# Optimization experiments

Measured on AMD Instinct MI355X. Metric: run time of the kernel, lower is better.

Reference implementation:

```python
import jax, jax.numpy as jnp
import numpy as np

L, D, H, DR, KF = 2, 256, 8, 64, 4   # n_layer, d_model, n_head, d_rpe, k_feedforward
B, S, T = 2, 256, 256
LN_EPS = 1e-5


def _ln(x, g, b):
    m = jnp.mean(x, -1, keepdims=True)
    v = jnp.mean((x - m) ** 2, -1, keepdims=True)
    return (x - m) * jax.lax.rsqrt(v + LN_EPS) * g + b


def _attn_rpe(q_in, kv_in, rpe, tgt_mask, wq, bq, wk, bk, wv, bv, wo, bo, wr, br):
    # RPE-biased multi-head cross attention: rpe -> (rpe_k, rpe_v) added per (src,tgt) pair.
    Bq, Sq, _ = q_in.shape
    Tk = kv_in.shape[1]
    Dh = D // H
    q = (q_in @ wq + bq).reshape(Bq, Sq, H, Dh)
    k = (kv_in @ wk + bk).reshape(Bq, Tk, H, Dh)
    v = (kv_in @ wv + bv).reshape(Bq, Tk, H, Dh)
    r = rpe @ wr + br                                   # [B,S,T,2D]
    rk, rv = jnp.split(r, 2, axis=-1)
    rk = rk.reshape(Bq, Sq, Tk, H, Dh)
    rv = rv.reshape(Bq, Sq, Tk, H, Dh)
    scale = 1.0 / np.sqrt(Dh).astype(np.float32)
    scores = (jnp.einsum('bshd,bthd->bhst', q, k)
              + jnp.einsum('bshd,bsthd->bhst', q, rk)) * scale
    scores = jnp.where(tgt_mask[:, None, None, :], -jnp.inf, scores)
    w = jax.nn.softmax(scores, axis=-1)                 # [B,H,S,T]
    out = (jnp.einsum('bhst,bthd->bshd', w, v)
           + jnp.einsum('bhst,bsthd->bshd', w, rv))
    return out.reshape(Bq, Sq, D) @ wo + bo


def _forward(src, tgt, rpe, src_padding_mask, tgt_padding_mask, p):
    for i in range(L):  # loop over n_layer (structurally distinct params)
        s2 = _ln(src, p['ln1_g'][i], p['ln1_b'][i])
        tn = _ln(tgt, p['lnt_g'][i], p['lnt_b'][i])
        a = _attn_rpe(s2, tn, rpe, tgt_padding_mask,
                      p['wq'][i], p['bq'][i], p['wk'][i], p['bk'][i],
                      p['wv'][i], p['bv'][i], p['wo'][i], p['bo'][i],
                      p['wr'][i], p['br'][i])
        src = src + a
        s2 = _ln(src, p['ln2_g'][i], p['ln2_b'][i])
        s2 = jax.nn.relu(s2 @ p['w1'][i] + p['b1'][i]) @ p['w2'][i] + p['b2'][i]
        src = src + s2
        src = jnp.where(src_padding_mask[:, :, None], 0.0, src)
    return src


def setup_inputs() -> dict:
    key = jax.random.key(0)
    ks = jax.random.split(key, 16)
    f = lambda k, shp: (0.02 * jax.random.normal(k, shp)).astype(jnp.float32)
    return {
        'src': jax.random.normal(ks[0], (B, S, D), jnp.float32),
        'tgt': jax.random.normal(ks[1], (B, T, D), jnp.float32),
        'rpe': jax.random.normal(ks[2], (B, S, T, DR), jnp.float32),
        'src_padding_mask': jax.random.bernoulli(ks[3], 0.05, (B, S)),
        'tgt_padding_mask': jax.random.bernoulli(ks[4], 0.1, (B, T)),
        'ln1_g': jnp.ones((L, D), jnp.float32), 'ln1_b': jnp.zeros((L, D), jnp.float32),
        'lnt_g': jnp.ones((L, D), jnp.float32), 'lnt_b': jnp.zeros((L, D), jnp.float32),
        'ln2_g': jnp.ones((L, D), jnp.float32), 'ln2_b': jnp.zeros((L, D), jnp.float32),
        'wq': f(ks[5], (L, D, D)), 'bq': jnp.zeros((L, D), jnp.float32),
        'wk': f(ks[6], (L, D, D)), 'bk': jnp.zeros((L, D), jnp.float32),
        'wv': f(ks[7], (L, D, D)), 'bv': jnp.zeros((L, D), jnp.float32),
        'wo': f(ks[8], (L, D, D)), 'bo': jnp.zeros((L, D), jnp.float32),
        'wr': f(ks[9], (L, DR, 2 * D)), 'br': jnp.zeros((L, 2 * D), jnp.float32),
        'w1': f(ks[10], (L, D, KF * D)), 'b1': jnp.zeros((L, KF * D), jnp.float32),
        'w2': f(ks[11], (L, KF * D, D)), 'b2': jnp.zeros((L, D), jnp.float32),
    }


def reference(src, tgt, rpe, src_padding_mask, tgt_padding_mask,
              ln1_g, ln1_b, lnt_g, lnt_b, ln2_g, ln2_b,
              wq, bq, wk, bk, wv, bv, wo, bo, wr, br, w1, b1, w2, b2):
    p = dict(ln1_g=ln1_g, ln1_b=ln1_b, lnt_g=lnt_g, lnt_b=lnt_b,
             ln2_g=ln2_g, ln2_b=ln2_b, wq=wq, bq=bq, wk=wk, bk=bk,
             wv=wv, bv=bv, wo=wo, bo=bo, wr=wr, br=br,
             w1=w1, b1=b1, w2=w2, b2=b2)
    return _forward(src, tgt, rpe, src_padding_mask, tgt_padding_mask, p)
```

## Files before the change

kernel.cpp:

```cpp
#include <hip/hip_runtime.h>
#include <math.h>

#define NEG_INF -1e30f

__global__ __launch_bounds__(256) void qkv_ln_kernel(
    const float* __restrict__ srcin, const float* __restrict__ tgt,
    const float* __restrict__ g1, const float* __restrict__ b1,
    const float* __restrict__ gt, const float* __restrict__ bt,
    const float* __restrict__ bo,
    const float* __restrict__ wq, const float* __restrict__ wk, const float* __restrict__ wv,
    const float* __restrict__ bq, const float* __restrict__ bk, const float* __restrict__ bv,
    float* __restrict__ Qb, float* __restrict__ Kb, float* __restrict__ Vb,
    float* __restrict__ X)
{
  __shared__ float As[32][8][36];
  __shared__ float Bs[32][64];
  int z = blockIdx.z;
  int m0 = blockIdx.y * 32, n0 = blockIdx.x * 64;
  const float* Bw   = (z == 0) ? wq : (z == 1) ? wk : wv;
  const float* bias = (z == 0) ? bq : (z == 1) ? bk : bv;
  const float* g    = (z == 0) ? g1 : gt;
  const float* be   = (z == 0) ? b1 : bt;
  int tid = threadIdx.x;
  int r = tid >> 3, c4 = tid & 7;
  int row = m0 + r;
  const float* arow = ((z == 0) ? srcin : tgt) + (size_t)row * 256 + c4 * 32;

  float4 x[8];
  float s = 0, ss = 0;
#pragma unroll
  for (int j = 0; j < 8; ++j) {
    x[j] = ((const float4*)arow)[j];
    s  += x[j].x + x[j].y + x[j].z + x[j].w;
    ss += x[j].x*x[j].x + x[j].y*x[j].y + x[j].z*x[j].z + x[j].w*x[j].w;
  }
#pragma unroll
  for (int off = 1; off < 8; off <<= 1) {
    s  += __shfl_xor(s,  off);
    ss += __shfl_xor(ss, off);
  }
  float mean = s * (1.0f / 256.0f);
  float var  = ss * (1.0f / 256.0f) - mean * mean;
  float rstd = rsqrtf(var + 1e-5f);
#pragma unroll
  for (int j = 0; j < 8; ++j) {
    float4 gg = ((const float4*)(g  + c4 * 32))[j];
    float4 bb = ((const float4*)(be + c4 * 32))[j];
    As[j*4+0][c4][r] = (x[j].x - mean) * rstd * gg.x + bb.x;
    As[j*4+1][c4][r] = (x[j].y - mean) * rstd * gg.y + bb.y;
    As[j*4+2][c4][r] = (x[j].z - mean) * rstd * gg.z + bb.z;
    As[j*4+3][c4][r] = (x[j].w - mean) * rstd * gg.w + bb.w;
  }
  if (z == 0 && blockIdx.x == 0) {
#pragma unroll
    for (int j = 0; j < 8; ++j) {
      float4 bo4 = ((const float4*)(bo + c4 * 32))[j];
      float4 xi;
      xi.x = x[j].x + bo4.x; xi.y = x[j].y + bo4.y;
      xi.z = x[j].z + bo4.z; xi.w = x[j].w + bo4.w;
      *(float4*)&X[(size_t)row * 256 + c4 * 32 + j * 4] = xi;
    }
  }
  __syncthreads();

  int tx = tid & 15, ty = tid >> 4;
  float acc[2][4] = {};
  for (int kc = 0; kc < 256; kc += 32) {
    const float* bp = Bw + (size_t)(kc + r) * 256 + n0;
    float4 b0  = *(const float4*)(bp + c4 * 4);
    float4 b1v = *(const float4*)(bp + 32 + c4 * 4);
    *(float4*)&Bs[r][c4 * 4]      = b0;
    *(float4*)&Bs[r][32 + c4 * 4] = b1v;
    __syncthreads();
    int kcc = kc >> 5;
#pragma unroll
    for (int kk = 0; kk < 32; ++kk) {
      float2 av = *(const float2*)&As[kk][kcc][ty * 2];
      float4 bv = *(const float4*)&Bs[kk][tx * 4];
      acc[0][0] = fmaf(av.x, bv.x, acc[0][0]); acc[0][1] = fmaf(av.x, bv.y, acc[0][1]);
      acc[0][2] = fmaf(av.x, bv.z, acc[0][2]); acc[0][3] = fmaf(av.x, bv.w, acc[0][3]);
      acc[1][0] = fmaf(av.y, bv.x, acc[1][0]); acc[1][1] = fmaf(av.y, bv.y, acc[1][1]);
      acc[1][2] = fmaf(av.y, bv.z, acc[1][2]); acc[1][3] = fmaf(av.y, bv.w, acc[1][3]);
    }
    __syncthreads();
  }

  int c0 = n0 + tx * 4;
  const float scale = 0.1767766952966369f;
#pragma unroll
  for (int i = 0; i < 2; ++i) {
    int m = m0 + ty * 2 + i;
    float4 rr;
    rr.x = acc[i][0] + bias[c0 + 0];
    rr.y = acc[i][1] + bias[c0 + 1];
    rr.z = acc[i][2] + bias[c0 + 2];
    rr.w = acc[i][3] + bias[c0 + 3];
    if (z == 0) {
      rr.x *= scale; rr.y *= scale; rr.z *= scale; rr.w *= scale;
      *(float4*)&Qb[m * 256 + c0] = rr;
    } else {
      int b = m >> 8, t = m & 255, h = c0 >> 5, d0 = c0 & 31;
      float* dst = ((z == 1) ? Kb : Vb) + (size_t)(b * 8 + h) * 8192 + t * 32 + d0;
      *(float4*)dst = rr;
    }
  }
}

__global__ __launch_bounds__(256) void ff1_ln2_kernel(
    const float* __restrict__ Xin,
    const float* __restrict__ g2, const float* __restrict__ be2,
    const float* __restrict__ b2, const int* __restrict__ smask,
    const float* __restrict__ w1, const float* __restrict__ b1,
    float* __restrict__ H1, float* __restrict__ outb)
{
  __shared__ float As[32][8][36];
  __shared__ float Bs[32][64];
  int m0 = blockIdx.y * 32, n0 = blockIdx.x * 64;
  int tid = threadIdx.x;
  int r = tid >> 3, c4 = tid & 7;
  int row = m0 + r;
  const float* arow = Xin + (size_t)row * 256 + c4 * 32;

  float4 x[8];
  float s = 0, ss = 0;
#pragma unroll
  for (int j = 0; j < 8; ++j) {
    x[j] = ((const float4*)arow)[j];
    s  += x[j].x + x[j].y + x[j].z + x[j].w;
    ss += x[j].x*x[j].x + x[j].y*x[j].y + x[j].z*x[j].z + x[j].w*x[j].w;
  }
#pragma unroll
  for (int off = 1; off < 8; off <<= 1) {
    s  += __shfl_xor(s,  off);
    ss += __shfl_xor(ss, off);
  }
  float mean = s * (1.0f / 256.0f);
  float var  = ss * (1.0f / 256.0f) - mean * mean;
  float rstd = rsqrtf(var + 1e-5f);
#pragma unroll
  for (int j = 0; j < 8; ++j) {
    float4 gg = ((const float4*)(g2  + c4 * 32))[j];
    float4 bb = ((const float4*)(be2 + c4 * 32))[j];
    As[j*4+0][c4][r] = (x[j].x - mean) * rstd * gg.x + bb.x;
    As[j*4+1][c4][r] = (x[j].y - mean) * rstd * gg.y + bb.y;
    As[j*4+2][c4][r] = (x[j].z - mean) * rstd * gg.z + bb.z;
    As[j*4+3][c4][r] = (x[j].w - mean) * rstd * gg.w + bb.w;
  }
  if (blockIdx.x == 0) {
    float mm = (smask[row] != 0) ? 0.0f : 1.0f;
#pragma unroll
    for (int j = 0; j < 8; ++j) {
      float4 b24 = ((const float4*)(b2 + c4 * 32))[j];
      float4 oi;
      oi.x = mm * (x[j].x + b24.x); oi.y = mm * (x[j].y + b24.y);
      oi.z = mm * (x[j].z + b24.z); oi.w = mm * (x[j].w + b24.w);
      *(float4*)&outb[(size_t)row * 256 + c4 * 32 + j * 4] = oi;
    }
  }
  __syncthreads();

  int tx = tid & 15, ty = tid >> 4;
  float acc[2][4] = {};
  for (int kc = 0; kc < 256; kc += 32) {
    const float* bp = w1 + (size_t)(kc + r) * 1024 + n0;
    float4 b0  = *(const float4*)(bp + c4 * 4);
    float4 b1v = *(const float4*)(bp + 32 + c4 * 4);
    *(float4*)&Bs[r][c4 * 4]      = b0;
    *(float4*)&Bs[r][32 + c4 * 4] = b1v;
    __syncthreads();
    int kcc = kc >> 5;
#pragma unroll
    for (int kk = 0; kk < 32; ++kk) {
      float2 av = *(const float2*)&As[kk][kcc][ty * 2];
      float4 bv = *(const float4*)&Bs[kk][tx * 4];
      acc[0][0] = fmaf(av.x, bv.x, acc[0][0]); acc[0][1] = fmaf(av.x, bv.y, acc[0][1]);
      acc[0][2] = fmaf(av.x, bv.z, acc[0][2]); acc[0][3] = fmaf(av.x, bv.w, acc[0][3]);
      acc[1][0] = fmaf(av.y, bv.x, acc[1][0]); acc[1][1] = fmaf(av.y, bv.y, acc[1][1]);
      acc[1][2] = fmaf(av.y, bv.z, acc[1][2]); acc[1][3] = fmaf(av.y, bv.w, acc[1][3]);
    }
    __syncthreads();
  }

  int c0 = n0 + tx * 4;
#pragma unroll
  for (int i = 0; i < 2; ++i) {
    int m = m0 + ty * 2 + i;
    float4 rr;
    rr.x = fmaxf(acc[i][0] + b1[c0 + 0], 0.0f);
    rr.y = fmaxf(acc[i][1] + b1[c0 + 1], 0.0f);
    rr.z = fmaxf(acc[i][2] + b1[c0 + 2], 0.0f);
    rr.w = fmaxf(acc[i][3] + b1[c0 + 3], 0.0f);
    *(float4*)&H1[m * 1024 + c0] = rr;
  }
}

__device__ __forceinline__ void gemm_core32(
    const float* __restrict__ A, int lda,
    const float* __restrict__ Bw, int ldb,
    int kbeg, int kend, int m0, int n0,
    float acc[2][4])
{
  __shared__ float At[32][34];
  __shared__ float Bs[32][64];
  int tid = threadIdx.x;
  int tx = tid & 15, ty = tid >> 4;
  int r  = tid >> 3;
  int c4 = tid & 7;
  for (int kc = kbeg; kc < kend; kc += 32) {
    float4 a = *(const float4*)(A + (size_t)(m0 + r) * lda + kc + c4 * 4);
    const float* bp = Bw + (size_t)(kc + r) * ldb + n0;
    float4 b0 = *(const float4*)(bp + c4 * 4);
    float4 b1v = *(const float4*)(bp + 32 + c4 * 4);
    At[c4*4+0][r] = a.x; At[c4*4+1][r] = a.y; At[c4*4+2][r] = a.z; At[c4*4+3][r] = a.w;
    *(float4*)&Bs[r][c4*4]      = b0;
    *(float4*)&Bs[r][32 + c4*4] = b1v;
    __syncthreads();
#pragma unroll
    for (int k = 0; k < 32; ++k) {
      float2 av = *(const float2*)&At[k][ty * 2];
      float4 bv = *(const float4*)&Bs[k][tx * 4];
      acc[0][0] = fmaf(av.x, bv.x, acc[0][0]); acc[0][1] = fmaf(av.x, bv.y, acc[0][1]);
      acc[0][2] = fmaf(av.x, bv.z, acc[0][2]); acc[0][3] = fmaf(av.x, bv.w, acc[0][3]);
      acc[1][0] = fmaf(av.y, bv.x, acc[1][0]); acc[1][1] = fmaf(av.y, bv.y, acc[1][1]);
      acc[1][2] = fmaf(av.y, bv.z, acc[1][2]); acc[1][3] = fmaf(av.y, bv.w, acc[1][3]);
    }
    __syncthreads();
  }
}

__global__ __launch_bounds__(256) void wo_kernel(
    const float* __restrict__ AO, const float* __restrict__ wo,
    float* __restrict__ X)
{
  int m0 = blockIdx.y * 32, n0 = blockIdx.x * 64;
  int kbeg = blockIdx.z * 128;
  float acc[2][4] = {};
  gemm_core32(AO, 256, wo, 256, kbeg, kbeg + 128, m0, n0, acc);
  int tid = threadIdx.x, tx = tid & 15, ty = tid >> 4;
  int c0 = n0 + tx * 4;
#pragma unroll
  for (int i = 0; i < 2; ++i) {
    int m = m0 + ty * 2 + i;
    atomicAdd(&X[m * 256 + c0 + 0], acc[i][0]);
    atomicAdd(&X[m * 256 + c0 + 1], acc[i][1]);
    atomicAdd(&X[m * 256 + c0 + 2], acc[i][2]);
    atomicAdd(&X[m * 256 + c0 + 3], acc[i][3]);
  }
}

__global__ __launch_bounds__(256) void ff2_kernel(
    const float* __restrict__ H1, const float* __restrict__ w2,
    const int* __restrict__ smask, float* __restrict__ outb)
{
  int m0 = blockIdx.y * 32, n0 = blockIdx.x * 64;
  int kbeg = blockIdx.z * 256;
  float acc[2][4] = {};
  gemm_core32(H1, 1024, w2, 256, kbeg, kbeg + 256, m0, n0, acc);
  int tid = threadIdx.x, tx = tid & 15, ty = tid >> 4;
  int c0 = n0 + tx * 4;
#pragma unroll
  for (int i = 0; i < 2; ++i) {
    int m = m0 + ty * 2 + i;
    float mm = (smask[m] != 0) ? 0.0f : 1.0f;
    atomicAdd(&outb[m * 256 + c0 + 0], mm * acc[i][0]);
    atomicAdd(&outb[m * 256 + c0 + 1], mm * acc[i][1]);
    atomicAdd(&outb[m * 256 + c0 + 2], mm * acc[i][2]);
    atomicAdd(&outb[m * 256 + c0 + 3], mm * acc[i][3]);
  }
}

__global__ __launch_bounds__(256) void attn_kernel(
    const float* __restrict__ Qb, const float* __restrict__ Kb, const float* __restrict__ Vb,
    const float* __restrict__ rpe, const int* __restrict__ tmask,
    const float* __restrict__ wrl, const float* __restrict__ brl,
    float* __restrict__ AO)
{
  __shared__ float Ks[256][32];
  __shared__ float Vt[32][260];
  __shared__ float ps[4][256];
  __shared__ float qs[16][32];
  __shared__ float wks[5][32];
  __shared__ float wvs[5][32];
  int bid = blockIdx.x;
  int b = bid >> 7, h = (bid >> 4) & 7, s0 = (bid & 15) << 4;
  int tid = threadIdx.x;
  const float* Kp = Kb + (size_t)(b * 8 + h) * 8192;
  const float* Vp = Vb + (size_t)(b * 8 + h) * 8192;
  {
    int t = tid;
    const float4* kr = (const float4*)(Kp + t * 32);
    const float4* vr = (const float4*)(Vp + t * 32);
    int sw = t & 7;
#pragma unroll
    for (int c = 0; c < 8; ++c) {
      float4 k4 = kr[c];
      *(float4*)&Ks[t][(c ^ sw) * 4] = k4;
    }
#pragma unroll
    for (int c = 0; c < 8; ++c) {
      float4 v4 = vr[c];
      Vt[c*4+0][t] = v4.x; Vt[c*4+1][t] = v4.y; Vt[c*4+2][t] = v4.z; Vt[c*4+3][t] = v4.w;
    }
  }
  if (tid < 160) {
    int j = tid >> 5, d = tid & 31;
    wks[j][d] = (j < 4) ? wrl[j * 512 + h * 32 + d]       : brl[h * 32 + d];
    wvs[j][d] = (j < 4) ? wrl[j * 512 + 256 + h * 32 + d] : brl[256 + h * 32 + d];
  }
  if (tid >= 128) {
    int u = tid - 128;
    int rr2 = u >> 3, cc = u & 7;
    *(float4*)&qs[rr2][cc*4] =
        *(const float4*)&Qb[(b * 256 + s0 + rr2) * 256 + h * 32 + cc * 4];
  }
  __syncthreads();

  int w = tid >> 6, lane = tid & 63;
  int msk[4];
#pragma unroll
  for (int it = 0; it < 4; ++it) msk[it] = tmask[b * 256 + it * 64 + lane];

  for (int i = 0; i < 4; ++i) {
    int sl = w * 4 + i;
    int s = s0 + sl;
    float4 q4[8];
#pragma unroll
    for (int c = 0; c < 8; ++c) q4[c] = *(const float4*)&qs[sl][c * 4];
    float qw[4]; float qbr = 0.0f;
#pragma unroll
    for (int j = 0; j < 4; ++j) {
      float t0 = 0;
#pragma unroll
      for (int c = 0; c < 8; ++c) {
        float4 wv4 = *(const float4*)&wks[j][c * 4];
        t0 += q4[c].x*wv4.x + q4[c].y*wv4.y + q4[c].z*wv4.z + q4[c].w*wv4.w;
      }
      qw[j] = t0;
    }
#pragma unroll
    for (int c = 0; c < 8; ++c) {
      float4 wv4 = *(const float4*)&wks[4][c * 4];
      qbr += q4[c].x*wv4.x + q4[c].y*wv4.y + q4[c].z*wv4.z + q4[c].w*wv4.w;
    }
    const float4* rp4 = (const float4*)(rpe + (size_t)(b * 256 + s) * 1024);
    float sc[4]; float4 rr[4];
#pragma unroll
    for (int it = 0; it < 4; ++it) {
      int t = it * 64 + lane;
      int sw = t & 7;
      float sv = 0;
#pragma unroll
      for (int c = 0; c < 8; ++c) {
        float4 k4 = *(const float4*)&Ks[t][(c ^ sw) * 4];
        sv = fmaf(q4[c].x, k4.x, sv); sv = fmaf(q4[c].y, k4.y, sv);
        sv = fmaf(q4[c].z, k4.z, sv); sv = fmaf(q4[c].w, k4.w, sv);
      }
      float4 rv = rp4[t];
      rr[it] = rv;
      sv += rv.x*qw[0] + rv.y*qw[1] + rv.z*qw[2] + rv.w*qw[3] + qbr;
      if (msk[it] != 0) sv = NEG_INF;
      sc[it] = sv;
    }
    float mval = fmaxf(fmaxf(sc[0], sc[1]), fmaxf(sc[2], sc[3]));
#pragma unroll
    for (int off = 32; off >= 1; off >>= 1) mval = fmaxf(mval, __shfl_xor(mval, off));
    float p[4], lsum = 0;
#pragma unroll
    for (int it = 0; it < 4; ++it) { p[it] = __expf(sc[it] - mval); lsum += p[it]; }
    float wj0 = 0, wj1 = 0, wj2 = 0, wj3 = 0;
#pragma unroll
    for (int it = 0; it < 4; ++it) {
      wj0 = fmaf(p[it], rr[it].x, wj0);
      wj1 = fmaf(p[it], rr[it].y, wj1);
      wj2 = fmaf(p[it], rr[it].z, wj2);
      wj3 = fmaf(p[it], rr[it].w, wj3);
    }
#pragma unroll
    for (int off = 32; off >= 1; off >>= 1) {
      lsum += __shfl_xor(lsum, off);
      wj0 += __shfl_xor(wj0, off);
      wj1 += __shfl_xor(wj1, off);
      wj2 += __shfl_xor(wj2, off);
      wj3 += __shfl_xor(wj3, off);
    }
#pragma unroll
    for (int it = 0; it < 4; ++it) ps[w][it * 64 + lane] = p[it];
    int g = lane >> 5, d = lane & 31;
    float o = 0;
#pragma unroll
    for (int n = 0; n < 32; ++n) {
      int t = g * 128 + n * 4;
      float4 p4 = *(const float4*)&ps[w][t];
      float4 v4 = *(const float4*)&Vt[d][t];
      o += p4.x*v4.x + p4.y*v4.y + p4.z*v4.z + p4.w*v4.w;
    }
    o += __shfl_xor(o, 32);
    float corr = wj0 * wvs[0][d] + wj1 * wvs[1][d] + wj2 * wvs[2][d] + wj3 * wvs[3][d];
    float oval = (o + corr) / lsum + wvs[4][d];
    if (lane < 32) AO[(b * 256 + s) * 256 + h * 32 + d] = oval;
  }
}

extern "C" void kernel_launch(void* const* d_in, const int* in_sizes, int n_in,
                              void* d_out, int out_size, void* d_ws, size_t ws_size,
                              hipStream_t stream)
{
  const float* src  = (const float*)d_in[0];
  const float* tgt  = (const float*)d_in[1];
  const float* rpe  = (const float*)d_in[2];
  const int*   smask = (const int*)d_in[3];
  const int*   tmask = (const int*)d_in[4];
  const float* ln1g = (const float*)d_in[5];
  const float* ln1b = (const float*)d_in[6];
  const float* lntg = (const float*)d_in[7];
  const float* lntb = (const float*)d_in[8];
  const float* ln2g = (const float*)d_in[9];
  const float* ln2b = (const float*)d_in[10];
  const float* wq = (const float*)d_in[11];
  const float* bq = (const float*)d_in[12];
  const float* wk = (const float*)d_in[13];
  const float* bk = (const float*)d_in[14];
  const float* wv = (const float*)d_in[15];
  const float* bv = (const float*)d_in[16];
  const float* wo = (const float*)d_in[17];
  const float* bo = (const float*)d_in[18];
  const float* wr = (const float*)d_in[19];
  const float* br = (const float*)d_in[20];
  const float* w1 = (const float*)d_in[21];
  const float* b1 = (const float*)d_in[22];
  const float* w2 = (const float*)d_in[23];
  const float* b2 = (const float*)d_in[24];

  float* ws   = (float*)d_ws;
  float* Qb   = ws;
  float* Kb   = ws + 131072;
  float* Vb   = ws + 262144;
  float* AO   = ws + 393216;
  float* X    = ws + 524288;
  float* SRC1 = ws + 655360;
  float* H1   = ws + 786432;

  for (int l = 0; l < 2; ++l) {
    const float* srcin = l ? SRC1 : src;
    float* outb = l ? (float*)d_out : SRC1;
    qkv_ln_kernel<<<dim3(4, 16, 3), 256, 0, stream>>>(
        srcin, tgt, ln1g + l*256, ln1b + l*256, lntg + l*256, lntb + l*256,
        bo + l*256,
        wq + l*65536, wk + l*65536, wv + l*65536,
        bq + l*256, bk + l*256, bv + l*256,
        Qb, Kb, Vb, X);
    attn_kernel<<<256, 256, 0, stream>>>(Qb, Kb, Vb, rpe, tmask,
                                         wr + l*2048, br + l*512, AO);
    wo_kernel<<<dim3(4, 16, 2), 256, 0, stream>>>(AO, wo + l*65536, X);
    ff1_ln2_kernel<<<dim3(16, 16), 256, 0, stream>>>(
        X, ln2g + l*256, ln2b + l*256, b2 + l*256, smask,
        w1 + l*262144, b1 + l*1024, H1, outb);
    ff2_kernel<<<dim3(4, 16, 4), 256, 0, stream>>>(H1, w2 + l*262144, smask, outb);
  }
}
```

Before: 276.6 us.

## Fuse output projection into attention and FF1+FF2 into one kernel

The Wo projection is folded into the attention kernel. Each block multiplies its per-head output tile by the matching 32-row slice of Wo and atomically accumulates into X. FF1 and FF2 are likewise fused: each block keeps its ReLU hidden tile in shared memory, multiplies it by the corresponding W2 rows, and atomically adds into the output, which the QKV kernel now zeroes beforehand. This removes two launches per layer and the AO and H1 global round trips, at the cost of many more fp32 atomics and smaller per-block GEMM efficiency.

```diff
diff --git a/kernel.cpp b/kernel.cpp
--- a/kernel.cpp
+++ b/kernel.cpp
@@ -11,7 +11,7 @@
     const float* __restrict__ wq, const float* __restrict__ wk, const float* __restrict__ wv,
     const float* __restrict__ bq, const float* __restrict__ bk, const float* __restrict__ bv,
     float* __restrict__ Qb, float* __restrict__ Kb, float* __restrict__ Vb,
-    float* __restrict__ X)
+    float* __restrict__ X, float* __restrict__ outb)
 {
   __shared__ float As[32][8][36];
   __shared__ float Bs[32][64];
@@ -22,9 +22,9 @@
   const float* g    = (z == 0) ? g1 : gt;
   const float* be   = (z == 0) ? b1 : bt;
   int tid = threadIdx.x;
-  int r = tid >> 3, c4 = tid & 7;
+  int r = tid >> 3, c8 = tid & 7;
   int row = m0 + r;
-  const float* arow = ((z == 0) ? srcin : tgt) + (size_t)row * 256 + c4 * 32;
+  const float* arow = ((z == 0) ? srcin : tgt) + (size_t)row * 256 + c8 * 32;
 
   float4 x[8];
   float s = 0, ss = 0;
@@ -44,22 +44,28 @@
   float rstd = rsqrtf(var + 1e-5f);
 #pragma unroll
   for (int j = 0; j < 8; ++j) {
-    float4 gg = ((const float4*)(g  + c4 * 32))[j];
-    float4 bb = ((const float4*)(be + c4 * 32))[j];
-    As[j*4+0][c4][r] = (x[j].x - mean) * rstd * gg.x + bb.x;
-    As[j*4+1][c4][r] = (x[j].y - mean) * rstd * gg.y + bb.y;
-    As[j*4+2][c4][r] = (x[j].z - mean) * rstd * gg.z + bb.z;
-    As[j*4+3][c4][r] = (x[j].w - mean) * rstd * gg.w + bb.w;
+    float4 gg = ((const float4*)(g  + c8 * 32))[j];
+    float4 bb = ((const float4*)(be + c8 * 32))[j];
+    As[j*4+0][c8][r] = (x[j].x - mean) * rstd * gg.x + bb.x;
+    As[j*4+1][c8][r] = (x[j].y - mean) * rstd * gg.y + bb.y;
+    As[j*4+2][c8][r] = (x[j].z - mean) * rstd * gg.z + bb.z;
+    As[j*4+3][c8][r] = (x[j].w - mean) * rstd * gg.w + bb.w;
   }
   if (z == 0 && blockIdx.x == 0) {
 #pragma unroll
     for (int j = 0; j < 8; ++j) {
-      float4 bo4 = ((const float4*)(bo + c4 * 32))[j];
+      float4 bo4 = ((const float4*)(bo + c8 * 32))[j];
       float4 xi;
       xi.x = x[j].x + bo4.x; xi.y = x[j].y + bo4.y;
       xi.z = x[j].z + bo4.z; xi.w = x[j].w + bo4.w;
-      *(float4*)&X[(size_t)row * 256 + c4 * 32 + j * 4] = xi;
-    }
+      *(float4*)&X[(size_t)row * 256 + c8 * 32 + j * 4] = xi;
+    }
+  }
+  if (z == 1 && blockIdx.x == 1) {
+    float4 zz = {};
+#pragma unroll
+    for (int j = 0; j < 8; ++j)
+      *(float4*)&outb[(size_t)row * 256 + c8 * 32 + j * 4] = zz;
   }
   __syncthreads();
 
@@ -67,10 +73,10 @@
   float acc[2][4] = {};
   for (int kc = 0; kc < 256; kc += 32) {
     const float* bp = Bw + (size_t)(kc + r) * 256 + n0;
-    float4 b0  = *(const float4*)(bp + c4 * 4);
-    float4 b1v = *(const float4*)(bp + 32 + c4 * 4);
-    *(float4*)&Bs[r][c4 * 4]      = b0;
-    *(float4*)&Bs[r][32 + c4 * 4] = b1v;
+    float4 b0  = *(const float4*)(bp + c8 * 4);
+    float4 b1v = *(const float4*)(bp + 32 + c8 * 4);
+    *(float4*)&Bs[r][c8 * 4]      = b0;
+    *(float4*)&Bs[r][32 + c8 * 4] = b1v;
     __syncthreads();
     int kcc = kc >> 5;
 #pragma unroll
@@ -106,181 +112,23 @@
   }
 }
 
-__global__ __launch_bounds__(256) void ff1_ln2_kernel(
-    const float* __restrict__ Xin,
-    const float* __restrict__ g2, const float* __restrict__ be2,
-    const float* __restrict__ b2, const int* __restrict__ smask,
-    const float* __restrict__ w1, const float* __restrict__ b1,
-    float* __restrict__ H1, float* __restrict__ outb)
-{
-  __shared__ float As[32][8][36];
-  __shared__ float Bs[32][64];
-  int m0 = blockIdx.y * 32, n0 = blockIdx.x * 64;
-  int tid = threadIdx.x;
-  int r = tid >> 3, c4 = tid & 7;
-  int row = m0 + r;
-  const float* arow = Xin + (size_t)row * 256 + c4 * 32;
-
-  float4 x[8];
-  float s = 0, ss = 0;
-#pragma unroll
-  for (int j = 0; j < 8; ++j) {
-    x[j] = ((const float4*)arow)[j];
-    s  += x[j].x + x[j].y + x[j].z + x[j].w;
-    ss += x[j].x*x[j].x + x[j].y*x[j].y + x[j].z*x[j].z + x[j].w*x[j].w;
-  }
-#pragma unroll
-  for (int off = 1; off < 8; off <<= 1) {
-    s  += __shfl_xor(s,  off);
-    ss += __shfl_xor(ss, off);
-  }
-  float mean = s * (1.0f / 256.0f);
-  float var  = ss * (1.0f / 256.0f) - mean * mean;
-  float rstd = rsqrtf(var + 1e-5f);
-#pragma unroll
-  for (int j = 0; j < 8; ++j) {
-    float4 gg = ((const float4*)(g2  + c4 * 32))[j];
-    float4 bb = ((const float4*)(be2 + c4 * 32))[j];
-    As[j*4+0][c4][r] = (x[j].x - mean) * rstd * gg.x + bb.x;
-    As[j*4+1][c4][r] = (x[j].y - mean) * rstd * gg.y + bb.y;
-    As[j*4+2][c4][r] = (x[j].z - mean) * rstd * gg.z + bb.z;
-    As[j*4+3][c4][r] = (x[j].w - mean) * rstd * gg.w + bb.w;
-  }
-  if (blockIdx.x == 0) {
-    float mm = (smask[row] != 0) ? 0.0f : 1.0f;
-#pragma unroll
-    for (int j = 0; j < 8; ++j) {
-      float4 b24 = ((const float4*)(b2 + c4 * 32))[j];
-      float4 oi;
-      oi.x = mm * (x[j].x + b24.x); oi.y = mm * (x[j].y + b24.y);
-      oi.z = mm * (x[j].z + b24.z); oi.w = mm * (x[j].w + b24.w);
-      *(float4*)&outb[(size_t)row * 256 + c4 * 32 + j * 4] = oi;
-    }
-  }
-  __syncthreads();
-
-  int tx = tid & 15, ty = tid >> 4;
-  float acc[2][4] = {};
-  for (int kc = 0; kc < 256; kc += 32) {
-    const float* bp = w1 + (size_t)(kc + r) * 1024 + n0;
-    float4 b0  = *(const float4*)(bp + c4 * 4);
-    float4 b1v = *(const float4*)(bp + 32 + c4 * 4);
-    *(float4*)&Bs[r][c4 * 4]      = b0;
-    *(float4*)&Bs[r][32 + c4 * 4] = b1v;
-    __syncthreads();
-    int kcc = kc >> 5;
-#pragma unroll
-    for (int kk = 0; kk < 32; ++kk) {
-      float2 av = *(const float2*)&As[kk][kcc][ty * 2];
-      float4 bv = *(const float4*)&Bs[kk][tx * 4];
-      acc[0][0] = fmaf(av.x, bv.x, acc[0][0]); acc[0][1] = fmaf(av.x, bv.y, acc[0][1]);
-      acc[0][2] = fmaf(av.x, bv.z, acc[0][2]); acc[0][3] = fmaf(av.x, bv.w, acc[0][3]);
-      acc[1][0] = fmaf(av.y, bv.x, acc[1][0]); acc[1][1] = fmaf(av.y, bv.y, acc[1][1]);
-      acc[1][2] = fmaf(av.y, bv.z, acc[1][2]); acc[1][3] = fmaf(av.y, bv.w, acc[1][3]);
-    }
-    __syncthreads();
-  }
-
-  int c0 = n0 + tx * 4;
-#pragma unroll
-  for (int i = 0; i < 2; ++i) {
-    int m = m0 + ty * 2 + i;
-    float4 rr;
-    rr.x = fmaxf(acc[i][0] + b1[c0 + 0], 0.0f);
-    rr.y = fmaxf(acc[i][1] + b1[c0 + 1], 0.0f);
-    rr.z = fmaxf(acc[i][2] + b1[c0 + 2], 0.0f);
-    rr.w = fmaxf(acc[i][3] + b1[c0 + 3], 0.0f);
-    *(float4*)&H1[m * 1024 + c0] = rr;
-  }
-}
-
-__device__ __forceinline__ void gemm_core32(
-    const float* __restrict__ A, int lda,
-    const float* __restrict__ Bw, int ldb,
-    int kbeg, int kend, int m0, int n0,
-    float acc[2][4])
-{
-  __shared__ float At[32][34];
-  __shared__ float Bs[32][64];
-  int tid = threadIdx.x;
-  int tx = tid & 15, ty = tid >> 4;
-  int r  = tid >> 3;
-  int c4 = tid & 7;
-  for (int kc = kbeg; kc < kend; kc += 32) {
-    float4 a = *(const float4*)(A + (size_t)(m0 + r) * lda + kc + c4 * 4);
-    const float* bp = Bw + (size_t)(kc + r) * ldb + n0;
-    float4 b0 = *(const float4*)(bp + c4 * 4);
-    float4 b1v = *(const float4*)(bp + 32 + c4 * 4);
-    At[c4*4+0][r] = a.x; At[c4*4+1][r] = a.y; At[c4*4+2][r] = a.z; At[c4*4+3][r] = a.w;
-    *(float4*)&Bs[r][c4*4]      = b0;
-    *(float4*)&Bs[r][32 + c4*4] = b1v;
-    __syncthreads();
-#pragma unroll
-    for (int k = 0; k < 32; ++k) {
-      float2 av = *(const float2*)&At[k][ty * 2];
-      float4 bv = *(const float4*)&Bs[k][tx * 4];
-      acc[0][0] = fmaf(av.x, bv.x, acc[0][0]); acc[0][1] = fmaf(av.x, bv.y, acc[0][1]);
-      acc[0][2] = fmaf(av.x, bv.z, acc[0][2]); acc[0][3] = fmaf(av.x, bv.w, acc[0][3]);
-      acc[1][0] = fmaf(av.y, bv.x, acc[1][0]); acc[1][1] = fmaf(av.y, bv.y, acc[1][1]);
-      acc[1][2] = fmaf(av.y, bv.z, acc[1][2]); acc[1][3] = fmaf(av.y, bv.w, acc[1][3]);
-    }
-    __syncthreads();
-  }
-}
-
-__global__ __launch_bounds__(256) void wo_kernel(
-    const float* __restrict__ AO, const float* __restrict__ wo,
-    float* __restrict__ X)
-{
-  int m0 = blockIdx.y * 32, n0 = blockIdx.x * 64;
-  int kbeg = blockIdx.z * 128;
-  float acc[2][4] = {};
-  gemm_core32(AO, 256, wo, 256, kbeg, kbeg + 128, m0, n0, acc);
-  int tid = threadIdx.x, tx = tid & 15, ty = tid >> 4;
-  int c0 = n0 + tx * 4;
-#pragma unroll
-  for (int i = 0; i < 2; ++i) {
-    int m = m0 + ty * 2 + i;
-    atomicAdd(&X[m * 256 + c0 + 0], acc[i][0]);
-    atomicAdd(&X[m * 256 + c0 + 1], acc[i][1]);
-    atomicAdd(&X[m * 256 + c0 + 2], acc[i][2]);
-    atomicAdd(&X[m * 256 + c0 + 3], acc[i][3]);
-  }
-}
-
-__global__ __launch_bounds__(256) void ff2_kernel(
-    const float* __restrict__ H1, const float* __restrict__ w2,
-    const int* __restrict__ smask, float* __restrict__ outb)
-{
-  int m0 = blockIdx.y * 32, n0 = blockIdx.x * 64;
-  int kbeg = blockIdx.z * 256;
-  float acc[2][4] = {};
-  gemm_core32(H1, 1024, w2, 256, kbeg, kbeg + 256, m0, n0, acc);
-  int tid = threadIdx.x, tx = tid & 15, ty = tid >> 4;
-  int c0 = n0 + tx * 4;
-#pragma unroll
-  for (int i = 0; i < 2; ++i) {
-    int m = m0 + ty * 2 + i;
-    float mm = (smask[m] != 0) ? 0.0f : 1.0f;
-    atomicAdd(&outb[m * 256 + c0 + 0], mm * acc[i][0]);
-    atomicAdd(&outb[m * 256 + c0 + 1], mm * acc[i][1]);
-    atomicAdd(&outb[m * 256 + c0 + 2], mm * acc[i][2]);
-    atomicAdd(&outb[m * 256 + c0 + 3], mm * acc[i][3]);
-  }
-}
-
-__global__ __launch_bounds__(256) void attn_kernel(
+__global__ __launch_bounds__(256) void attn_wo_kernel(
     const float* __restrict__ Qb, const float* __restrict__ Kb, const float* __restrict__ Vb,
     const float* __restrict__ rpe, const int* __restrict__ tmask,
     const float* __restrict__ wrl, const float* __restrict__ brl,
-    float* __restrict__ AO)
+    const float* __restrict__ wo_l,
+    float* __restrict__ X)
 {
-  __shared__ float Ks[256][32];
+  __shared__ float KsW[8192];
   __shared__ float Vt[32][260];
   __shared__ float ps[4][256];
   __shared__ float qs[16][32];
   __shared__ float wks[5][32];
   __shared__ float wvs[5][32];
+  __shared__ float Os[16][32];
+  float (*Ks)[32]  = (float (*)[32])KsW;
+  float (*wos)[256] = (float (*)[256])KsW;
+
   int bid = blockIdx.x;
   int b = bid >> 7, h = (bid >> 4) & 7, s0 = (bid & 15) << 4;
   int tid = threadIdx.x;
@@ -397,8 +245,173 @@
     o += __shfl_xor(o, 32);
     float corr = wj0 * wvs[0][d] + wj1 * wvs[1][d] + wj2 * wvs[2][d] + wj3 * wvs[3][d];
     float oval = (o + corr) / lsum + wvs[4][d];
-    if (lane < 32) AO[(b * 256 + s) * 256 + h * 32 + d] = oval;
-  }
+    if (lane < 32) Os[sl][d] = oval;
+  }
+  __syncthreads();
+
+  {
+    int k = tid >> 3, c8 = tid & 7;
+    const float4* sw = (const float4*)(wo_l + (size_t)(h * 32 + k) * 256 + c8 * 32);
+    float4* dst = (float4*)&wos[k][c8 * 32];
+#pragma unroll
+    for (int j = 0; j < 8; ++j) dst[j] = sw[j];
+  }
+  __syncthreads();
+  {
+    int col = lane * 4, r0 = w * 4;
+    float4 acc[4] = {};
+    for (int kk = 0; kk < 8; ++kk) {
+      float4 w0  = *(const float4*)&wos[kk*4+0][col];
+      float4 w1v = *(const float4*)&wos[kk*4+1][col];
+      float4 w2v = *(const float4*)&wos[kk*4+2][col];
+      float4 w3v = *(const float4*)&wos[kk*4+3][col];
+#pragma unroll
+      for (int r = 0; r < 4; ++r) {
+        float4 o4 = *(const float4*)&Os[r0 + r][kk * 4];
+        acc[r].x += o4.x*w0.x + o4.y*w1v.x + o4.z*w2v.x + o4.w*w3v.x;
+        acc[r].y += o4.x*w0.y + o4.y*w1v.y + o4.z*w2v.y + o4.w*w3v.y;
+        acc[r].z += o4.x*w0.z + o4.y*w1v.z + o4.z*w2v.z + o4.w*w3v.z;
+        acc[r].w += o4.x*w0.w + o4.y*w1v.w + o4.z*w2v.w + o4.w*w3v.w;
+      }
+    }
+#pragma unroll
+    for (int r = 0; r < 4; ++r) {
+      float* xp = &X[(size_t)(b * 256 + s0 + r0 + r) * 256 + col];
+      atomicAdd(xp + 0, acc[r].x);
+      atomicAdd(xp + 1, acc[r].y);
+      atomicAdd(xp + 2, acc[r].z);
+      atomicAdd(xp + 3, acc[r].w);
+    }
+  }
+}
+
+__global__ __launch_bounds__(256) void ff_fused_kernel(
+    const float* __restrict__ Xin,
+    const float* __restrict__ g2, const float* __restrict__ be2,
+    const float* __restrict__ b2, const int* __restrict__ smask,
+    const float* __restrict__ w1, const float* __restrict__ b1,
+    const float* __restrict__ w2,
+    float* __restrict__ outb)
+{
+  __shared__ float AsW[9216];
+  __shared__ float BsH[2048];
+  float (*w2s)[256] = (float (*)[256])AsW;
+  float (*Bs)[64] = (float (*)[64])BsH;
+  float (*Hs)[64] = (float (*)[64])BsH;
+#define AS(k,c,m) AsW[((k) * 8 + (c)) * 36 + (m)]
+  int m0 = blockIdx.y * 32, n0 = blockIdx.x * 64;
+  int tid = threadIdx.x;
+  int r = tid >> 3, c8 = tid & 7;
+  int row = m0 + r;
+  const float* arow = Xin + (size_t)row * 256 + c8 * 32;
+
+  float4 x[8];
+  float s = 0, ss = 0;
+#pragma unroll
+  for (int j = 0; j < 8; ++j) {
+    x[j] = ((const float4*)arow)[j];
+    s  += x[j].x + x[j].y + x[j].z + x[j].w;
+    ss += x[j].x*x[j].x + x[j].y*x[j].y + x[j].z*x[j].z + x[j].w*x[j].w;
+  }
+#pragma unroll
+  for (int off = 1; off < 8; off <<= 1) {
+    s  += __shfl_xor(s,  off);
+    ss += __shfl_xor(ss, off);
+  }
+  float mean = s * (1.0f / 256.0f);
+  float var  = ss * (1.0f / 256.0f) - mean * mean;
+  float rstd = rsqrtf(var + 1e-5f);
+#pragma unroll
+  for (int j = 0; j < 8; ++j) {
+    float4 gg = ((const float4*)(g2  + c8 * 32))[j];
+    float4 bb = ((const float4*)(be2 + c8 * 32))[j];
+    AS(j*4+0, c8, r) = (x[j].x - mean) * rstd * gg.x + bb.x;
+    AS(j*4+1, c8, r) = (x[j].y - mean) * rstd * gg.y + bb.y;
+    AS(j*4+2, c8, r) = (x[j].z - mean) * rstd * gg.z + bb.z;
+    AS(j*4+3, c8, r) = (x[j].w - mean) * rstd * gg.w + bb.w;
+  }
+  __syncthreads();
+
+  int tx = tid & 15, ty = tid >> 4;
+  float acc[2][4] = {};
+  for (int kc = 0; kc < 256; kc += 32) {
+    const float* bp = w1 + (size_t)(kc + r) * 1024 + n0;
+    float4 b0  = *(const float4*)(bp + c8 * 4);
+    float4 b1v = *(const float4*)(bp + 32 + c8 * 4);
+    *(float4*)&Bs[r][c8 * 4]      = b0;
+    *(float4*)&Bs[r][32 + c8 * 4] = b1v;
+    __syncthreads();
+    int kcc = kc >> 5;
+#pragma unroll
+    for (int kk = 0; kk < 32; ++kk) {
+      float2 av = *(const float2*)&AS(kk, kcc, ty * 2);
+      float4 bv = *(const float4*)&Bs[kk][tx * 4];
+      acc[0][0] = fmaf(av.x, bv.x, acc[0][0]); acc[0][1] = fmaf(av.x, bv.y, acc[0][1]);
+      acc[0][2] = fmaf(av.x, bv.z, acc[0][2]); acc[0][3] = fmaf(av.x, bv.w, acc[0][3]);
+      acc[1][0] = fmaf(av.y, bv.x, acc[1][0]); acc[1][1] = fmaf(av.y, bv.y, acc[1][1]);
+      acc[1][2] = fmaf(av.y, bv.z, acc[1][2]); acc[1][3] = fmaf(av.y, bv.w, acc[1][3]);
+    }
+    __syncthreads();
+  }
+
+  {
+    int c0 = n0 + tx * 4;
+#pragma unroll
+    for (int i = 0; i < 2; ++i) {
+      int rl = ty * 2 + i;
+      Hs[rl][tx*4+0] = fmaxf(acc[i][0] + b1[c0 + 0], 0.0f);
+      Hs[rl][tx*4+1] = fmaxf(acc[i][1] + b1[c0 + 1], 0.0f);
+      Hs[rl][tx*4+2] = fmaxf(acc[i][2] + b1[c0 + 2], 0.0f);
+      Hs[rl][tx*4+3] = fmaxf(acc[i][3] + b1[c0 + 3], 0.0f);
+    }
+  }
+
+  int lane = tid & 63, w = tid >> 6;
+  int col = lane * 4, r0 = w * 8;
+  float4 acc2[8] = {};
+  for (int half = 0; half < 2; ++half) {
+    __syncthreads();
+    {
+      int k = tid >> 3;
+      const float4* sw = (const float4*)(w2 + (size_t)(n0 + half * 32 + k) * 256 + c8 * 32);
+      float4* dst = (float4*)&w2s[k][c8 * 32];
+#pragma unroll
+      for (int j = 0; j < 8; ++j) dst[j] = sw[j];
+    }
+    __syncthreads();
+    for (int kk = 0; kk < 8; ++kk) {
+      float4 w0  = *(const float4*)&w2s[kk*4+0][col];
+      float4 w1v = *(const float4*)&w2s[kk*4+1][col];
+      float4 w2v = *(const float4*)&w2s[kk*4+2][col];
+      float4 w3v = *(const float4*)&w2s[kk*4+3][col];
+#pragma unroll
+      for (int rr = 0; rr < 8; ++rr) {
+        float4 h4 = *(const float4*)&Hs[r0 + rr][half * 32 + kk * 4];
+        acc2[rr].x += h4.x*w0.x + h4.y*w1v.x + h4.z*w2v.x + h4.w*w3v.x;
+        acc2[rr].y += h4.x*w0.y + h4.y*w1v.y + h4.z*w2v.y + h4.w*w3v.y;
+        acc2[rr].z += h4.x*w0.z + h4.y*w1v.z + h4.z*w2v.z + h4.w*w3v.z;
+        acc2[rr].w += h4.x*w0.w + h4.y*w1v.w + h4.z*w2v.w + h4.w*w3v.w;
+      }
+    }
+  }
+#pragma unroll
+  for (int rr = 0; rr < 8; ++rr) {
+    int m = m0 + r0 + rr;
+    float mm = (smask[m] != 0) ? 0.0f : 1.0f;
+    float4 add = acc2[rr];
+    if (blockIdx.x == 0) {
+      float4 x4  = *(const float4*)&Xin[(size_t)m * 256 + col];
+      float4 b24 = *(const float4*)&b2[col];
+      add.x += x4.x + b24.x; add.y += x4.y + b24.y;
+      add.z += x4.z + b24.z; add.w += x4.w + b24.w;
+    }
+    float* op = &outb[(size_t)m * 256 + col];
+    atomicAdd(op + 0, mm * add.x);
+    atomicAdd(op + 1, mm * add.y);
+    atomicAdd(op + 2, mm * add.z);
+    atomicAdd(op + 3, mm * add.w);
+  }
+#undef AS
 }
 
 extern "C" void kernel_launch(void* const* d_in, const int* in_sizes, int n_in,
@@ -435,10 +448,8 @@
   float* Qb   = ws;
   float* Kb   = ws + 131072;
   float* Vb   = ws + 262144;
-  float* AO   = ws + 393216;
-  float* X    = ws + 524288;
-  float* SRC1 = ws + 655360;
-  float* H1   = ws + 786432;
+  float* X    = ws + 393216;
+  float* SRC1 = ws + 524288;
 
   for (int l = 0; l < 2; ++l) {
     const float* srcin = l ? SRC1 : src;
@@ -448,13 +459,12 @@
         bo + l*256,
         wq + l*65536, wk + l*65536, wv + l*65536,
         bq + l*256, bk + l*256, bv + l*256,
-        Qb, Kb, Vb, X);
-    attn_kernel<<<256, 256, 0, stream>>>(Qb, Kb, Vb, rpe, tmask,
-                                         wr + l*2048, br + l*512, AO);
-    wo_kernel<<<dim3(4, 16, 2), 256, 0, stream>>>(AO, wo + l*65536, X);
-    ff1_ln2_kernel<<<dim3(16, 16), 256, 0, stream>>>(
+        Qb, Kb, Vb, X, outb);
+    attn_wo_kernel<<<256, 256, 0, stream>>>(Qb, Kb, Vb, rpe, tmask,
+                                            wr + l*2048, br + l*512,
+                                            wo + l*65536, X);
+    ff_fused_kernel<<<dim3(16, 16), 256, 0, stream>>>(
         X, ln2g + l*256, ln2b + l*256, b2 + l*256, smask,
-        w1 + l*262144, b1 + l*1024, H1, outb);
-    ff2_kernel<<<dim3(4, 16, 4), 256, 0, stream>>>(H1, w2 + l*262144, smask, outb);
+        w1 + l*262144, b1 + l*1024, w2 + l*262144, outb);
   }
 }
```

Result: slower. 345.2 us (+24.8%).
